# Optimization experiments

Hardware: AMD Instinct MI355X
Metric: run time of the kernel (lower is better)

Reference implementation:

```python
import jax, jax.numpy as jnp
import numpy as np

N_NODES = 50000
N_EDGES = 800000
IN_CH = 128
OUT_CH = 64
HEADS = 2
NEG_SLOPE = 0.2


def _gat_conv(x, src, dst, W, a_src, a_dst, b, n):
    """PyG-style GATConv (eval mode: no dropout), self-loops already appended.
    x: [n, F_in]; W: [F_in, H*C]; a_src/a_dst: [H, C]; b: [H*C]."""
    H, C = a_src.shape
    h = (x @ W).reshape(n, H, C)                       # [n, H, C]
    alpha_src = jnp.sum(h * a_src, axis=-1)            # [n, H]
    alpha_dst = jnp.sum(h * a_dst, axis=-1)            # [n, H]
    e = alpha_src[src] + alpha_dst[dst]                # [E, H]
    e = jnp.where(e > 0, e, NEG_SLOPE * e)             # LeakyReLU(0.2)
    # neighbor-wise (destination-grouped) softmax, numerically stable
    m = jax.ops.segment_max(e, dst, num_segments=n)
    e = jnp.exp(e - m[dst])
    denom = jax.ops.segment_sum(e, dst, num_segments=n)
    alpha = e / (denom[dst] + 1e-16)                   # [E, H]
    out = jax.ops.segment_sum(alpha[:, :, None] * h[src], dst, num_segments=n)
    return out.reshape(n, H * C) + b


def setup_inputs() -> dict:
    key = jax.random.key(0)
    ks = jax.random.split(key, 12)
    s = 0.08  # glorot-ish scale
    x = jax.random.normal(ks[0], (N_NODES, IN_CH), dtype=jnp.float32)
    edge_index = jax.random.randint(ks[1], (2, N_EDGES), 0, N_NODES, dtype=jnp.int64)
    H, O = HEADS, OUT_CH
    return {
        "x": x,
        "edge_index": edge_index,
        "W1": jax.random.normal(ks[2], (IN_CH, H * 2 * O), dtype=jnp.float32) * s,
        "a_src1": jax.random.normal(ks[3], (H, 2 * O), dtype=jnp.float32) * s,
        "a_dst1": jax.random.normal(ks[4], (H, 2 * O), dtype=jnp.float32) * s,
        "b1": jnp.zeros((H * 2 * O,), dtype=jnp.float32),
        "W_mu": jax.random.normal(ks[5], (2 * O * H, H * O), dtype=jnp.float32) * s,
        "a_src_mu": jax.random.normal(ks[6], (H, O), dtype=jnp.float32) * s,
        "a_dst_mu": jax.random.normal(ks[7], (H, O), dtype=jnp.float32) * s,
        "b_mu": jnp.zeros((H * O,), dtype=jnp.float32),
        "W_ls": jax.random.normal(ks[8], (2 * O * H, H * O), dtype=jnp.float32) * s,
        "a_src_ls": jax.random.normal(ks[9], (H, O), dtype=jnp.float32) * s,
        "a_dst_ls": jax.random.normal(ks[10], (H, O), dtype=jnp.float32) * s,
        "b_ls": jnp.zeros((H * O,), dtype=jnp.float32),
    }


def reference(x, edge_index, W1, a_src1, a_dst1, b1,
              W_mu, a_src_mu, a_dst_mu, b_mu,
              W_ls, a_src_ls, a_dst_ls, b_ls):
    n = x.shape[0]
    loop = jnp.arange(n, dtype=edge_index.dtype)
    src = jnp.concatenate([edge_index[0], loop])  # PyG add_self_loops=True
    dst = jnp.concatenate([edge_index[1], loop])
    x1 = jax.nn.elu(_gat_conv(x, src, dst, W1, a_src1, a_dst1, b1, n))
    mu = _gat_conv(x1, src, dst, W_mu, a_src_mu, a_dst_mu, b_mu, n)
    logstd = _gat_conv(x1, src, dst, W_ls, a_src_ls, a_dst_ls, b_ls, n)
    return (mu, logstd)
```

## Files before the change

kernel.cpp:

```cpp
#include <hip/hip_runtime.h>


typedef unsigned short u16;
typedef unsigned int u32;
typedef _Float16 f16;
typedef f16 f16x8 __attribute__((ext_vector_type(8)));
typedef float f32x4v __attribute__((ext_vector_type(4)));

__device__ __forceinline__ u16 f2h(float f) {
    union { f16 h; u16 u; } t;
    t.h = (f16)f;
    return t.u;
}
__device__ __forceinline__ float4 loadh4(const u16* __restrict__ p, size_t i) {
    union { uint2 u; f16 h[4]; } t;
    t.u = *(const uint2*)(p + i);
    return make_float4((float)t.h[0], (float)t.h[1], (float)t.h[2], (float)t.h[3]);
}
__device__ __forceinline__ void store4(float* __restrict__ p, size_t i, float4 v) {
    *(float4*)(p + i) = v;
}
__device__ __forceinline__ void store4(u16* __restrict__ p, size_t i, float4 v) {
    union { uint2 u; f16 h[4]; } t;
    t.h[0] = (f16)v.x; t.h[1] = (f16)v.y; t.h[2] = (f16)v.z; t.h[3] = (f16)v.w;
    *(uint2*)(p + i) = t.u;
}

__global__ __launch_bounds__(256) void k_detect(const u32* __restrict__ ebuf,
                                                int* __restrict__ flag) {
    __shared__ int nz;
    if (threadIdx.x == 0) nz = 0;
    __syncthreads();
    if (ebuf[2 * threadIdx.x + 1] != 0u) atomicAdd(&nz, 1);
    __syncthreads();
    if (threadIdx.x == 0) *flag = (nz == 0) ? 1 : 0;
}

__global__ __launch_bounds__(256) void k_extract(const u32* __restrict__ ebuf, int E,
                                                 const int* __restrict__ flag,
                                                 int* __restrict__ se,
                                                 int* __restrict__ de,
                                                 int* __restrict__ deg) {
    int e = blockIdx.x * 256 + threadIdx.x;
    if (e >= E) return;
    int s, d;
    if (*flag) {
        s = (int)ebuf[2 * (size_t)e];
        d = (int)ebuf[2 * ((size_t)E + (size_t)e)];
    } else {
        s = (int)ebuf[e];
        d = (int)ebuf[(size_t)E + (size_t)e];
    }
    se[e] = s;
    de[e] = d;
    atomicAdd(&deg[d], 1);
}

__global__ __launch_bounds__(256) void k_scan_a(const int* __restrict__ deg, int n,
                                                int* __restrict__ bsum) {
    __shared__ int s[256];
    int i = blockIdx.x * 256 + threadIdx.x;
    s[threadIdx.x] = (i < n) ? deg[i] : 0;
    __syncthreads();
    for (int st = 128; st > 0; st >>= 1) {
        if (threadIdx.x < st) s[threadIdx.x] += s[threadIdx.x + st];
        __syncthreads();
    }
    if (threadIdx.x == 0) bsum[blockIdx.x] = s[0];
}

__global__ __launch_bounds__(256) void k_scan_b(int* __restrict__ bsum, int nb) {
    __shared__ int s[256];
    int t = threadIdx.x;
    int v = (t < nb) ? bsum[t] : 0;
    s[t] = v;
    __syncthreads();
    for (int off = 1; off < 256; off <<= 1) {
        int add = (t >= off) ? s[t - off] : 0;
        __syncthreads();
        s[t] += add;
        __syncthreads();
    }
    if (t < nb) bsum[t] = s[t] - v;
}

__global__ __launch_bounds__(256) void k_scan_c(const int* __restrict__ deg, int n,
                                                const int* __restrict__ bsum,
                                                int* __restrict__ rowptr,
                                                int* __restrict__ cursor, int E) {
    __shared__ int s[256];
    int t = threadIdx.x;
    int i = blockIdx.x * 256 + t;
    int v = (i < n) ? deg[i] : 0;
    s[t] = v;
    __syncthreads();
    for (int off = 1; off < 256; off <<= 1) {
        int add = (t >= off) ? s[t - off] : 0;
        __syncthreads();
        s[t] += add;
        __syncthreads();
    }
    if (i < n) {
        int ex = bsum[blockIdx.x] + s[t] - v;
        rowptr[i] = ex;
        cursor[i] = ex;
    }
    if (i == 0) rowptr[n] = E;
}

__global__ __launch_bounds__(256) void k_fill(const int* __restrict__ src,
                                              const int* __restrict__ dst, int E,
                                              int* __restrict__ cursor,
                                              int* __restrict__ csr_src) {
    int e = blockIdx.x * 256 + threadIdx.x;
    if (e < E) {
        int d = dst[e];
        int slot = atomicAdd(&cursor[d], 1);
        csr_src[slot] = src[e];
    }
}

__global__ __launch_bounds__(256) void k_cvt(const float* __restrict__ in,
                                             u16* __restrict__ out, int nElem) {
    int i = (blockIdx.x * 256 + threadIdx.x) * 4;
    if (i >= nElem) return;
    float4 v = *(const float4*)(in + i);
    store4(out, i, v);
}

__global__ __launch_bounds__(256) void k_tw(const float* __restrict__ Wl,
                                            const float* __restrict__ Wr, int split,
                                            int K, u16* __restrict__ Wt) {
    int idx = blockIdx.x * 256 + threadIdx.x;
    if (idx >= 256 * K) return;
    int c = idx / K, k = idx - c * K;
    float v;
    if (split == 256)
        v = Wl[(size_t)k * 256 + c];
    else
        v = (c < 128) ? Wl[(size_t)k * 128 + c] : Wr[(size_t)k * 128 + (c - 128)];
    Wt[idx] = f2h(v);
}

template <int K>
__global__ __launch_bounds__(64) void k_gemm_mfma(const u16* __restrict__ Ah,
                                                  const u16* __restrict__ Wt,
                                                  u16* __restrict__ out, int M) {
    const int lane = threadIdx.x;
    const int r0 = blockIdx.x * 16;
    const int li = lane & 15;
    const int quad = lane >> 4;
    int row = r0 + li;
    if (row >= M) row = M - 1;
    const u16* arow = Ah + (size_t)row * K + quad * 8;

    f32x4v acc[16];
#pragma unroll
    for (int ct = 0; ct < 16; ct++) acc[ct] = (f32x4v)(0.f);

    for (int t = 0; t < K; t += 32) {
        f16x8 a = *(const f16x8*)(arow + t);
#pragma unroll
        for (int ct = 0; ct < 16; ct++) {
            const u16* brow = Wt + (size_t)(ct * 16 + li) * K + t + quad * 8;
            f16x8 b = *(const f16x8*)brow;
            acc[ct] = __builtin_amdgcn_mfma_f32_16x16x32_f16(a, b, acc[ct], 0, 0, 0);
        }
    }

#pragma unroll
    for (int reg = 0; reg < 4; reg++) {
        int grow = r0 + quad * 4 + reg;
        if (grow < M) {
            u16* orow = out + (size_t)grow * 256 + li;
#pragma unroll
            for (int ct = 0; ct < 16; ct++) orow[ct * 16] = f2h(acc[ct][reg]);
        }
    }
}

template <int LOGW>
__global__ __launch_bounds__(256) void k_alphas(const u16* __restrict__ h,
                                                const float* __restrict__ as_lo,
                                                const float* __restrict__ as_hi,
                                                const float* __restrict__ ad_lo,
                                                const float* __restrict__ ad_hi,
                                                float* __restrict__ as_out,
                                                float* __restrict__ ad_out, int n) {
    const int W = 1 << LOGW;
    const int NS = 64 >> LOGW;
    int wid = blockIdx.x * 4 + (threadIdx.x >> 6);
    int lane = threadIdx.x & 63;
    if (wid >= n) return;
    int c = lane * 4;
    int ci = c & 127;
    const float* ap = (c < 128) ? as_lo : as_hi;
    const float* dp = (c < 128) ? ad_lo : ad_hi;
    float4 hv = loadh4(h, (size_t)wid * 256 + c);
    float4 av = *(const float4*)(ap + ci);
    float4 dv = *(const float4*)(dp + ci);
    float ssum = hv.x * av.x + hv.y * av.y + hv.z * av.z + hv.w * av.w;
    float dsum = hv.x * dv.x + hv.y * dv.y + hv.z * dv.z + hv.w * dv.w;
#pragma unroll
    for (int m = W / 2; m >= 1; m >>= 1) {
        ssum += __shfl_xor(ssum, m, 64);
        dsum += __shfl_xor(dsum, m, 64);
    }
    if ((lane & (W - 1)) == 0) {
        int slot = lane >> LOGW;
        as_out[(size_t)wid * NS + slot] = ssum;
        ad_out[(size_t)wid * NS + slot] = dsum;
    }
}

template <int LOGW, int MODE, typename OT>
__global__ __launch_bounds__(256) void k_agg(const u16* __restrict__ h,
                                             const int* __restrict__ rowptr,
                                             const int* __restrict__ csr_src,
                                             const float* __restrict__ as,
                                             const float* __restrict__ ad,
                                             const float* __restrict__ b_lo,
                                             const float* __restrict__ b_hi,
                                             OT* __restrict__ outp, int n) {
    const int NS = 64 >> LOGW;
    int wid = blockIdx.x * 4 + (threadIdx.x >> 6);
    int lane = threadIdx.x & 63;
    if (wid >= n) return;
    int slot = lane >> LOGW;
    int c = lane * 4;

    float adv = ad[(size_t)wid * NS + slot];
    float e = as[(size_t)wid * NS + slot] + adv;
    e = fmaxf(e, 0.2f * e);
    float w = __expf(e);
    float denom = w;
    float4 hv = loadh4(h, (size_t)wid * 256 + c);
    float acc0 = w * hv.x, acc1 = w * hv.y, acc2 = w * hv.z, acc3 = w * hv.w;

    const int rb = rowptr[wid], re = rowptr[wid + 1];
    int p = rb;
    for (; p + 4 <= re; p += 4) {
        int s0 = csr_src[p], s1 = csr_src[p + 1];
        int s2 = csr_src[p + 2], s3 = csr_src[p + 3];
        float e0 = as[(size_t)s0 * NS + slot] + adv;
        float e1 = as[(size_t)s1 * NS + slot] + adv;
        float e2 = as[(size_t)s2 * NS + slot] + adv;
        float e3 = as[(size_t)s3 * NS + slot] + adv;
        e0 = fmaxf(e0, 0.2f * e0);
        e1 = fmaxf(e1, 0.2f * e1);
        e2 = fmaxf(e2, 0.2f * e2);
        e3 = fmaxf(e3, 0.2f * e3);
        float w0 = __expf(e0), w1 = __expf(e1), w2 = __expf(e2), w3 = __expf(e3);
        float4 h0 = loadh4(h, (size_t)s0 * 256 + c);
        float4 h1 = loadh4(h, (size_t)s1 * 256 + c);
        float4 h2 = loadh4(h, (size_t)s2 * 256 + c);
        float4 h3 = loadh4(h, (size_t)s3 * 256 + c);
        denom += (w0 + w1) + (w2 + w3);
        acc0 += w0 * h0.x + w1 * h1.x + w2 * h2.x + w3 * h3.x;
        acc1 += w0 * h0.y + w1 * h1.y + w2 * h2.y + w3 * h3.y;
        acc2 += w0 * h0.z + w1 * h1.z + w2 * h2.z + w3 * h3.z;
        acc3 += w0 * h0.w + w1 * h1.w + w2 * h2.w + w3 * h3.w;
    }
    for (; p < re; ++p) {
        int s = csr_src[p];
        float ev = as[(size_t)s * NS + slot] + adv;
        ev = fmaxf(ev, 0.2f * ev);
        float ww = __expf(ev);
        denom += ww;
        float4 hh = loadh4(h, (size_t)s * 256 + c);
        acc0 += ww * hh.x;
        acc1 += ww * hh.y;
        acc2 += ww * hh.z;
        acc3 += ww * hh.w;
    }
    float inv = 1.0f / (denom + 1e-16f);

    int ci = c & 127;
    const float* bp = (c < 128) ? b_lo : b_hi;
    float4 bv = *(const float4*)(bp + ci);
    float v0 = acc0 * inv + bv.x;
    float v1 = acc1 * inv + bv.y;
    float v2 = acc2 * inv + bv.z;
    float v3 = acc3 * inv + bv.w;

    if (MODE == 0) {
        v0 = v0 > 0.f ? v0 : expm1f(v0);
        v1 = v1 > 0.f ? v1 : expm1f(v1);
        v2 = v2 > 0.f ? v2 : expm1f(v2);
        v3 = v3 > 0.f ? v3 : expm1f(v3);
        store4(outp, (size_t)wid * 256 + c, make_float4(v0, v1, v2, v3));
    } else {
        size_t base = (c < 128) ? ((size_t)wid * 128 + c)
                                : ((size_t)n * 128 + (size_t)wid * 128 + (c - 128));
        store4(outp, base, make_float4(v0, v1, v2, v3));
    }
}

extern "C" void kernel_launch(void* const* d_in, const int* in_sizes, int n_in,
                              void* d_out, int out_size, void* d_ws, size_t ws_size,
                              hipStream_t stream) {
    const float* x = (const float*)d_in[0];
    const u32* ebuf = (const u32*)d_in[1];
    const float* W1 = (const float*)d_in[2];
    const float* a_src1 = (const float*)d_in[3];
    const float* a_dst1 = (const float*)d_in[4];
    const float* b1 = (const float*)d_in[5];
    const float* W_mu = (const float*)d_in[6];
    const float* a_src_mu = (const float*)d_in[7];
    const float* a_dst_mu = (const float*)d_in[8];
    const float* b_mu = (const float*)d_in[9];
    const float* W_ls = (const float*)d_in[10];
    const float* a_src_ls = (const float*)d_in[11];
    const float* a_dst_ls = (const float*)d_in[12];
    const float* b_ls = (const float*)d_in[13];

    const int n = in_sizes[0] / 128;
    const int E = in_sizes[1] / 2;

    char* base = (char*)d_ws;
    size_t off = 0;
    auto alloc = [&](size_t b) -> char* {
        char* p = base + off;
        off = (off + b + 255) & ~(size_t)255;
        return p;
    };
    int* rowptr = (int*)alloc((size_t)(n + 1) * 4);
    int* cursor = (int*)alloc((size_t)n * 4);
    int* csr = (int*)alloc((size_t)E * 4);
    int* bsum = (int*)alloc(256 * 4);
    int* eflag = (int*)alloc(256);
    int* se = (int*)alloc((size_t)E * 4);
    int* de = (int*)alloc((size_t)E * 4);
    float* as = (float*)alloc((size_t)n * 4 * 4);
    float* ad = (float*)alloc((size_t)n * 4 * 4);
    u16* W1t = (u16*)alloc(256 * 128 * 2);
    u16* Wt2 = (u16*)alloc(256 * 256 * 2);
    u16* x1h = (u16*)alloc((size_t)n * 256 * 2);
    u16* xh = x1h;
    u16* h = (u16*)alloc((size_t)n * 256 * 2);

    const int nb = (n + 255) / 256;
    const int eg = (E + 255) / 256;
    const int ng4 = (n + 3) / 4;
    const int gm = (n + 15) / 16;

    hipMemsetAsync(cursor, 0, (size_t)n * 4, stream);
    k_detect<<<1, 256, 0, stream>>>(ebuf, eflag);
    k_extract<<<eg, 256, 0, stream>>>(ebuf, E, eflag, se, de, cursor);
    k_scan_a<<<nb, 256, 0, stream>>>(cursor, n, bsum);
    k_scan_b<<<1, 256, 0, stream>>>(bsum, nb);
    k_scan_c<<<nb, 256, 0, stream>>>(cursor, n, bsum, rowptr, cursor, E);
    k_fill<<<eg, 256, 0, stream>>>(se, de, E, cursor, csr);

    k_cvt<<<(n * 128 / 4 + 255) / 256, 256, 0, stream>>>(x, xh, n * 128);
    k_tw<<<(256 * 128 + 255) / 256, 256, 0, stream>>>(W1, W1, 256, 128, W1t);
    k_tw<<<(256 * 256 + 255) / 256, 256, 0, stream>>>(W_mu, W_ls, 128, 256, Wt2);

    k_gemm_mfma<128><<<gm, 64, 0, stream>>>(xh, W1t, h, n);
    k_alphas<5><<<ng4, 256, 0, stream>>>(h, a_src1, a_src1 + 128, a_dst1,
                                         a_dst1 + 128, as, ad, n);
    k_agg<5, 0, u16><<<ng4, 256, 0, stream>>>(h, rowptr, csr, as, ad, b1, b1 + 128,
                                              x1h, n);

    k_gemm_mfma<256><<<gm, 64, 0, stream>>>(x1h, Wt2, h, n);
    k_alphas<4><<<ng4, 256, 0, stream>>>(h, a_src_mu, a_src_ls, a_dst_mu, a_dst_ls,
                                         as, ad, n);
    k_agg<4, 1, float><<<ng4, 256, 0, stream>>>(h, rowptr, csr, as, ad, b_mu, b_ls,
                                                (float*)d_out, n);
}
```

Before: 438.4 us.

## Fuse attention-logit computation into MFMA GEMM epilogue and stage weights in LDS

Removes the separate k_alphas kernels by computing the per-head source and destination attention dot products in the GEMM epilogue from the fp32 accumulators, using cross-lane shuffles within each 16-lane group. The GEMM blocks grow from one to four waves, and each K-step's weight tile is staged into padded shared memory so the four waves share it instead of each reading it from global memory. This saves two launches and two re-reads of h, at the cost of extra syncthreads per K step and higher register pressure in the epilogue. As a side effect, the logits now come from fp32 accumulators rather than fp16-rounded h.

```diff
diff --git a/kernel.cpp b/kernel.cpp
--- a/kernel.cpp
+++ b/kernel.cpp
@@ -142,28 +142,46 @@
     Wt[idx] = f2h(v);
 }
 
-template <int K>
-__global__ __launch_bounds__(64) void k_gemm_mfma(const u16* __restrict__ Ah,
-                                                  const u16* __restrict__ Wt,
-                                                  u16* __restrict__ out, int M) {
-    const int lane = threadIdx.x;
-    const int r0 = blockIdx.x * 16;
+template <int K, int ALOGW>
+__global__ __launch_bounds__(256) void k_gemm_mfma(
+    const u16* __restrict__ Ah, const u16* __restrict__ Wt, u16* __restrict__ out,
+    float* __restrict__ as_out, float* __restrict__ ad_out,
+    const float* __restrict__ alo, const float* __restrict__ ahi,
+    const float* __restrict__ dlo, const float* __restrict__ dhi, int M) {
+    __shared__ u16 Bs[256 * 40];
+    const int tid = threadIdx.x;
+    const int wave = tid >> 6;
+    const int lane = tid & 63;
     const int li = lane & 15;
     const int quad = lane >> 4;
-    int row = r0 + li;
-    if (row >= M) row = M - 1;
-    const u16* arow = Ah + (size_t)row * K + quad * 8;
+    const int r0 = blockIdx.x * 64 + wave * 16;
+    int arowi = r0 + li;
+    if (arowi >= M) arowi = M - 1;
+    const u16* arow = Ah + (size_t)arowi * K + quad * 8;
 
     f32x4v acc[16];
 #pragma unroll
     for (int ct = 0; ct < 16; ct++) acc[ct] = (f32x4v)(0.f);
 
     for (int t = 0; t < K; t += 32) {
+        __syncthreads();
+        {
+            const u16* src = Wt + (size_t)tid * K + t;
+            u16* dst = Bs + tid * 40;
+            uint4 v0 = ((const uint4*)src)[0];
+            uint4 v1 = ((const uint4*)src)[1];
+            uint4 v2 = ((const uint4*)src)[2];
+            uint4 v3 = ((const uint4*)src)[3];
+            ((uint4*)dst)[0] = v0;
+            ((uint4*)(dst + 8))[0] = v1;
+            ((uint4*)(dst + 16))[0] = v2;
+            ((uint4*)(dst + 24))[0] = v3;
+        }
+        __syncthreads();
         f16x8 a = *(const f16x8*)(arow + t);
 #pragma unroll
         for (int ct = 0; ct < 16; ct++) {
-            const u16* brow = Wt + (size_t)(ct * 16 + li) * K + t + quad * 8;
-            f16x8 b = *(const f16x8*)brow;
+            f16x8 b = *(const f16x8*)(Bs + (ct * 16 + li) * 40 + quad * 8);
             acc[ct] = __builtin_amdgcn_mfma_f32_16x16x32_f16(a, b, acc[ct], 0, 0, 0);
         }
     }
@@ -177,39 +195,42 @@
             for (int ct = 0; ct < 16; ct++) orow[ct * 16] = f2h(acc[ct][reg]);
         }
     }
-}
-
-template <int LOGW>
-__global__ __launch_bounds__(256) void k_alphas(const u16* __restrict__ h,
-                                                const float* __restrict__ as_lo,
-                                                const float* __restrict__ as_hi,
-                                                const float* __restrict__ ad_lo,
-                                                const float* __restrict__ ad_hi,
-                                                float* __restrict__ as_out,
-                                                float* __restrict__ ad_out, int n) {
-    const int W = 1 << LOGW;
-    const int NS = 64 >> LOGW;
-    int wid = blockIdx.x * 4 + (threadIdx.x >> 6);
-    int lane = threadIdx.x & 63;
-    if (wid >= n) return;
-    int c = lane * 4;
-    int ci = c & 127;
-    const float* ap = (c < 128) ? as_lo : as_hi;
-    const float* dp = (c < 128) ? ad_lo : ad_hi;
-    float4 hv = loadh4(h, (size_t)wid * 256 + c);
-    float4 av = *(const float4*)(ap + ci);
-    float4 dv = *(const float4*)(dp + ci);
-    float ssum = hv.x * av.x + hv.y * av.y + hv.z * av.z + hv.w * av.w;
-    float dsum = hv.x * dv.x + hv.y * dv.y + hv.z * dv.z + hv.w * dv.w;
-#pragma unroll
-    for (int m = W / 2; m >= 1; m >>= 1) {
-        ssum += __shfl_xor(ssum, m, 64);
-        dsum += __shfl_xor(dsum, m, 64);
-    }
-    if ((lane & (W - 1)) == 0) {
-        int slot = lane >> LOGW;
-        as_out[(size_t)wid * NS + slot] = ssum;
-        ad_out[(size_t)wid * NS + slot] = dsum;
+
+    const int NS = 64 >> ALOGW;
+    const int SH = ALOGW - 2;
+    float aw[16], dw[16];
+#pragma unroll
+    for (int ct = 0; ct < 16; ct++) {
+        int col = ct * 16 + li;
+        aw[ct] = (col < 128) ? alo[col] : ahi[col - 128];
+        dw[ct] = (col < 128) ? dlo[col] : dhi[col - 128];
+    }
+#pragma unroll
+    for (int reg = 0; reg < 4; reg++) {
+        float s[4] = {0.f, 0.f, 0.f, 0.f};
+        float d[4] = {0.f, 0.f, 0.f, 0.f};
+#pragma unroll
+        for (int ct = 0; ct < 16; ct++) {
+            int sl = ct >> SH;
+            s[sl] += acc[ct][reg] * aw[ct];
+            d[sl] += acc[ct][reg] * dw[ct];
+        }
+#pragma unroll
+        for (int sl = 0; sl < NS; sl++) {
+#pragma unroll
+            for (int m = 1; m <= 8; m <<= 1) {
+                s[sl] += __shfl_xor(s[sl], m, 64);
+                d[sl] += __shfl_xor(d[sl], m, 64);
+            }
+        }
+        int grow = r0 + quad * 4 + reg;
+        if (li == 0 && grow < M) {
+#pragma unroll
+            for (int sl = 0; sl < NS; sl++) {
+                as_out[(size_t)grow * NS + sl] = s[sl];
+                ad_out[(size_t)grow * NS + sl] = d[sl];
+            }
+        }
     }
 }
 
@@ -342,7 +363,7 @@
     const int nb = (n + 255) / 256;
     const int eg = (E + 255) / 256;
     const int ng4 = (n + 3) / 4;
-    const int gm = (n + 15) / 16;
+    const int gg = (n + 63) / 64;
 
     hipMemsetAsync(cursor, 0, (size_t)n * 4, stream);
     k_detect<<<1, 256, 0, stream>>>(ebuf, eflag);
@@ -356,15 +377,14 @@
     k_tw<<<(256 * 128 + 255) / 256, 256, 0, stream>>>(W1, W1, 256, 128, W1t);
     k_tw<<<(256 * 256 + 255) / 256, 256, 0, stream>>>(W_mu, W_ls, 128, 256, Wt2);
 
-    k_gemm_mfma<128><<<gm, 64, 0, stream>>>(xh, W1t, h, n);
-    k_alphas<5><<<ng4, 256, 0, stream>>>(h, a_src1, a_src1 + 128, a_dst1,
-                                         a_dst1 + 128, as, ad, n);
+    k_gemm_mfma<128, 5><<<gg, 256, 0, stream>>>(xh, W1t, h, as, ad, a_src1,
+                                                a_src1 + 128, a_dst1, a_dst1 + 128,
+                                                n);
     k_agg<5, 0, u16><<<ng4, 256, 0, stream>>>(h, rowptr, csr, as, ad, b1, b1 + 128,
                                               x1h, n);
 
-    k_gemm_mfma<256><<<gm, 64, 0, stream>>>(x1h, Wt2, h, n);
-    k_alphas<4><<<ng4, 256, 0, stream>>>(h, a_src_mu, a_src_ls, a_dst_mu, a_dst_ls,
-                                         as, ad, n);
+    k_gemm_mfma<256, 4><<<gg, 256, 0, stream>>>(x1h, Wt2, h, as, ad, a_src_mu,
+                                                a_src_ls, a_dst_mu, a_dst_ls, n);
     k_agg<4, 1, float><<<ng4, 256, 0, stream>>>(h, rowptr, csr, as, ad, b_mu, b_ls,
                                                 (float*)d_out, n);
 }
```

After: 384.0 us. 12.4% less time.
